# Kernel optimization log

Measured on AMD Instinct MI355X. Metric: run time of the kernel, lower is better.

## Reference

```python
import jax, jax.numpy as jnp
import numpy as np

B, N, E, ENT, D, H, L = 64, 2048, 32768, 100000, 256, 256, 512


def setup_inputs() -> dict:
    key = jax.random.key(0)
    ks = jax.random.split(key, 12)
    return {
        "neighbors": jax.random.randint(ks[0], (B, N), 0, ENT),
        "adj_row": jax.random.randint(ks[1], (B, E), 0, N),
        "adj_col": jax.random.randint(ks[2], (B, E), 0, N),
        "adj_val": jax.random.uniform(ks[3], (B, E), dtype=jnp.float32),
        "emb_table": jax.random.normal(ks[4], (ENT, D), dtype=jnp.float32),
        "W1": jax.random.normal(ks[5], (D, H), dtype=jnp.float32) * (1.0 / np.sqrt(H)),
        "b1": jax.random.normal(ks[6], (H,), dtype=jnp.float32) * 0.01,
        "W2": jax.random.normal(ks[7], (H, H), dtype=jnp.float32) * (1.0 / np.sqrt(H)),
        "b2": jax.random.normal(ks[8], (H,), dtype=jnp.float32) * 0.01,
        "fc1_w": jax.random.normal(ks[9], (H, H), dtype=jnp.float32) * (1.0 / np.sqrt(H)),
        "fc1_b": jax.random.normal(ks[10], (H,), dtype=jnp.float32) * 0.01,
        "cur_len": L,
    }


def _gcn_layer(x, W, b, adj_row, adj_col, adj_val):
    # x: [B,N,din] -> support: [B,N,dout]
    support = jnp.einsum("bnd,dh->bnh", x, W)
    # sparse adj @ support: gather columns, scale by edge value, scatter-add to rows
    gathered = jnp.take_along_axis(support, adj_col[:, :, None], axis=1)  # [B,E,h]
    weighted = gathered * adj_val[:, :, None]
    agg = jax.vmap(lambda r, g: jax.ops.segment_sum(g, r, num_segments=N))(adj_row, weighted)
    return agg + b


def reference(neighbors, adj_row, adj_col, adj_val, emb_table, W1, b1, W2, b2, fc1_w, fc1_b, cur_len):
    x = emb_table[neighbors]                                   # [B,N,D] embedding gather
    x = _gcn_layer(x, W1, b1, adj_row, adj_col, adj_val)       # GCN layer 1
    x = _gcn_layer(x, W2, b2, adj_row, adj_col, adj_val)       # GCN layer 2
    seq = x[:, :cur_len, :]                                    # keep cur_node prefix, padded to common L
    pooled = jnp.mean(seq, axis=1, keepdims=True)              # self.seq == 'mean'
    return jax.nn.relu(jnp.einsum("blh,ho->blo", pooled, fc1_w) + fc1_b)  # [B,1,H]
```

## Files before the change

kernel.cpp:

```cpp
#include <hip/hip_runtime.h>

#define B 64
#define N 2048
#define E 32768
#define D 256
#define H 256
#define GCH 32
#define SEG 8
#define EPB (E / SEG)

__global__ __launch_bounds__(512) void edge_w_kernel(
    const int* __restrict__ adj_row, const int* __restrict__ adj_col,
    const float* __restrict__ adj_val, const int* __restrict__ cur_len,
    float* __restrict__ w_part, float* __restrict__ sw_part)
{
    __shared__ float wloc[N];
    __shared__ float sred[8];
    const int b = blockIdx.x, seg = blockIdx.y, tid = threadIdx.x;
    const int L = *cur_len;

    ((float4*)wloc)[tid] = make_float4(0.f, 0.f, 0.f, 0.f);
    __syncthreads();

    const int base = b * E + seg * EPB;
    const int4*   row4 = (const int4*)  (adj_row + base);
    const int4*   col4 = (const int4*)  (adj_col + base);
    const float4* val4 = (const float4*)(adj_val + base);

    float svp = 0.f;
    #pragma unroll
    for (int k = 0; k < EPB / (512 * 4); ++k) {
        const int    i = tid + k * 512;
        const int4   r = row4[i];
        const int4   c = col4[i];
        const float4 v = val4[i];
        if (r.x < L) { atomicAdd(&wloc[c.x], v.x); svp += v.x; }
        if (r.y < L) { atomicAdd(&wloc[c.y], v.y); svp += v.y; }
        if (r.z < L) { atomicAdd(&wloc[c.z], v.z); svp += v.z; }
        if (r.w < L) { atomicAdd(&wloc[c.w], v.w); svp += v.w; }
    }
    __syncthreads();

    float4* dst = (float4*)(w_part + ((size_t)b * SEG + seg) * N);
    dst[tid] = ((const float4*)wloc)[tid];

    for (int off = 32; off; off >>= 1) svp += __shfl_down(svp, off, 64);
    if ((tid & 63) == 0) sred[tid >> 6] = svp;
    __syncthreads();
    if (tid == 0) {
        float s = 0.f;
        #pragma unroll
        for (int i = 0; i < 8; ++i) s += sred[i];
        sw_part[b * SEG + seg] = s;
    }
}

__global__ __launch_bounds__(512) void edge_z_kernel(
    const int* __restrict__ adj_row, const int* __restrict__ adj_col,
    const float* __restrict__ adj_val, const float* __restrict__ w_part,
    float* __restrict__ z_part)
{
    __shared__ float wfull[N];
    __shared__ float zloc[N];
    const int b = blockIdx.x, seg = blockIdx.y, tid = threadIdx.x;

    const float4* wp4 = (const float4*)(w_part + (size_t)b * SEG * N);
    float4 s = make_float4(0.f, 0.f, 0.f, 0.f);
    #pragma unroll
    for (int sg = 0; sg < SEG; ++sg) {
        const float4 v = wp4[sg * (N / 4) + tid];
        s.x += v.x; s.y += v.y; s.z += v.z; s.w += v.w;
    }
    ((float4*)wfull)[tid] = s;
    ((float4*)zloc)[tid]  = make_float4(0.f, 0.f, 0.f, 0.f);
    __syncthreads();

    const int base = b * E + seg * EPB;
    const int4*   row4 = (const int4*)  (adj_row + base);
    const int4*   col4 = (const int4*)  (adj_col + base);
    const float4* val4 = (const float4*)(adj_val + base);

    #pragma unroll
    for (int k = 0; k < EPB / (512 * 4); ++k) {
        const int    i = tid + k * 512;
        const int4   r = row4[i];
        const int4   c = col4[i];
        const float4 v = val4[i];
        float wv;
        wv = wfull[r.x]; if (wv != 0.f) atomicAdd(&zloc[c.x], wv * v.x);
        wv = wfull[r.y]; if (wv != 0.f) atomicAdd(&zloc[c.y], wv * v.y);
        wv = wfull[r.z]; if (wv != 0.f) atomicAdd(&zloc[c.z], wv * v.z);
        wv = wfull[r.w]; if (wv != 0.f) atomicAdd(&zloc[c.w], wv * v.w);
    }
    __syncthreads();

    float4* dst = (float4*)(z_part + ((size_t)b * SEG + seg) * N);
    dst[tid] = ((const float4*)zloc)[tid];
}

__global__ __launch_bounds__(256) void gather_kernel(
    const int* __restrict__ neighbors, const float* __restrict__ emb,
    const float* __restrict__ z_part, float* __restrict__ u_part)
{
    const int b = blockIdx.x, grp = blockIdx.y, tid = threadIdx.x;
    const int lane = tid & 63, rg = tid >> 6;
    const int n0 = grp * 64;

    __shared__ float zh[2][64];
    __shared__ int   ns[64];
    if (tid < 128) {
        const int j = tid & 63, half = tid >> 6;
        float s = 0.f;
        #pragma unroll
        for (int sg = 0; sg < SEG / 2; ++sg)
            s += z_part[((size_t)b * SEG + half * (SEG / 2) + sg) * N + n0 + j];
        zh[half][j] = s;
        if (half == 0) ns[j] = neighbors[(size_t)b * N + n0 + j];
    }
    __syncthreads();

    const float4* __restrict__ emb4 = (const float4*)emb;
    float4 a0 = make_float4(0.f,0.f,0.f,0.f), a1 = a0, a2 = a0, a3 = a0;

    #pragma unroll
    for (int i = 0; i < 16; ++i) {
        const int j = i * 4 + rg;
        const float zv = zh[0][j] + zh[1][j];
        const size_t idx = (size_t)ns[j];
        const float4 v = emb4[idx * (D / 4) + lane];
        if ((i & 3) == 0)      { a0.x += zv*v.x; a0.y += zv*v.y; a0.z += zv*v.z; a0.w += zv*v.w; }
        else if ((i & 3) == 1) { a1.x += zv*v.x; a1.y += zv*v.y; a1.z += zv*v.z; a1.w += zv*v.w; }
        else if ((i & 3) == 2) { a2.x += zv*v.x; a2.y += zv*v.y; a2.z += zv*v.z; a2.w += zv*v.w; }
        else                   { a3.x += zv*v.x; a3.y += zv*v.y; a3.z += zv*v.z; a3.w += zv*v.w; }
    }
    float4 acc = make_float4(a0.x+a1.x+a2.x+a3.x, a0.y+a1.y+a2.y+a3.y,
                             a0.z+a1.z+a2.z+a3.z, a0.w+a1.w+a2.w+a3.w);

    __shared__ float4 red[256];
    red[tid] = acc;
    __syncthreads();
    if (tid < 64) {
        float4 a = red[tid], bb = red[tid + 64], c = red[tid + 128], d = red[tid + 192];
        float4 s = make_float4(a.x + bb.x + c.x + d.x, a.y + bb.y + c.y + d.y,
                               a.z + bb.z + c.z + d.z, a.w + bb.w + c.w + d.w);
        ((float4*)u_part)[((size_t)b * GCH + grp) * (D / 4) + tid] = s;
    }
}

__global__ __launch_bounds__(1024) void head_kernel(
    const float* __restrict__ u_part, const float* __restrict__ sw_part,
    const float* __restrict__ W1, const float* __restrict__ b1,
    const float* __restrict__ W2, const float* __restrict__ b2,
    const float* __restrict__ fc1_w, const float* __restrict__ fc1_b,
    const int* __restrict__ cur_len, float* __restrict__ out)
{
    const int b = blockIdx.x;
    const int t = threadIdx.x & 255;
    const int s = threadIdx.x >> 8;
    __shared__ float red[4][256];
    __shared__ float su[D];
    __shared__ float sy[H];
    __shared__ float sp[H];

    float part = 0.f;
    #pragma unroll
    for (int c = 0; c < GCH / 4; ++c)
        part += u_part[((size_t)b * GCH + s * (GCH / 4) + c) * D + t];
    red[s][t] = part;
    __syncthreads();
    if (s == 0) su[t] = red[0][t] + red[1][t] + red[2][t] + red[3][t];
    __syncthreads();

    part = 0.f;
    #pragma unroll 8
    for (int k = 0; k < 64; ++k) {
        const int d = s * 64 + k;
        part += su[d] * W1[d * H + t];
    }
    red[s][t] = part;
    __syncthreads();
    if (s == 0) {
        float sw = 0.f;
        #pragma unroll
        for (int i = 0; i < SEG; ++i) sw += sw_part[b * SEG + i];
        sy[t] = red[0][t] + red[1][t] + red[2][t] + red[3][t] + sw * b1[t];
    }
    __syncthreads();

    const float invL = 1.f / (float)(*cur_len);
    part = 0.f;
    #pragma unroll 8
    for (int k = 0; k < 64; ++k) {
        const int d = s * 64 + k;
        part += sy[d] * W2[d * H + t];
    }
    red[s][t] = part;
    __syncthreads();
    if (s == 0)
        sp[t] = (red[0][t] + red[1][t] + red[2][t] + red[3][t]) * invL + b2[t];
    __syncthreads();

    part = 0.f;
    #pragma unroll 8
    for (int k = 0; k < 64; ++k) {
        const int d = s * 64 + k;
        part += sp[d] * fc1_w[d * H + t];
    }
    red[s][t] = part;
    __syncthreads();
    if (s == 0) {
        const float v = red[0][t] + red[1][t] + red[2][t] + red[3][t] + fc1_b[t];
        out[(size_t)b * H + t] = fmaxf(v, 0.f);
    }
}

extern "C" void kernel_launch(void* const* d_in, const int* in_sizes, int n_in,
                              void* d_out, int out_size, void* d_ws, size_t ws_size,
                              hipStream_t stream) {
    const int*   neighbors = (const int*)  d_in[0];
    const int*   adj_row   = (const int*)  d_in[1];
    const int*   adj_col   = (const int*)  d_in[2];
    const float* adj_val   = (const float*)d_in[3];
    const float* emb_table = (const float*)d_in[4];
    const float* W1        = (const float*)d_in[5];
    const float* b1        = (const float*)d_in[6];
    const float* W2        = (const float*)d_in[7];
    const float* b2        = (const float*)d_in[8];
    const float* fc1_w     = (const float*)d_in[9];
    const float* fc1_b     = (const float*)d_in[10];
    const int*   cur_len   = (const int*)  d_in[11];
    float*       out       = (float*)d_out;

    float* wp_ws = (float*)d_ws;
    float* zp_ws = wp_ws + (size_t)B * SEG * N;
    float* sw_ws = zp_ws + (size_t)B * SEG * N;
    float* u_ws  = sw_ws + (size_t)B * SEG;

    edge_w_kernel<<<dim3(B, SEG), 512, 0, stream>>>(adj_row, adj_col, adj_val,
                                                    cur_len, wp_ws, sw_ws);
    edge_z_kernel<<<dim3(B, SEG), 512, 0, stream>>>(adj_row, adj_col, adj_val,
                                                    wp_ws, zp_ws);
    gather_kernel<<<dim3(B, GCH), 256, 0, stream>>>(neighbors, emb_table, zp_ws, u_ws);
    head_kernel<<<B, 1024, 0, stream>>>(u_ws, sw_ws, W1, b1, W2, b2,
                                        fc1_w, fc1_b, cur_len, out);
}
```

Measured before the change: 222.2 us.

## Fuse edge weight and edge aggregation passes into one block per batch

Merges the two edge kernels into a single kernel in which one 1024-thread block per batch computes the row-masked column weights in shared memory and then the second-hop aggregation. This removes the per-segment partial buffers, their global reduction and one kernel launch, and simplifies the gather and head kernels. In exchange the edge work runs on only 64 blocks instead of 512, which reduces parallelism across the GPU's compute units.

```diff
diff --git a/kernel.cpp b/kernel.cpp
--- a/kernel.cpp
+++ b/kernel.cpp
@@ -6,31 +6,32 @@
 #define D 256
 #define H 256
 #define GCH 32
-#define SEG 8
-#define EPB (E / SEG)
-
-__global__ __launch_bounds__(512) void edge_w_kernel(
+
+__global__ __launch_bounds__(1024) void edges_fused_kernel(
     const int* __restrict__ adj_row, const int* __restrict__ adj_col,
     const float* __restrict__ adj_val, const int* __restrict__ cur_len,
-    float* __restrict__ w_part, float* __restrict__ sw_part)
+    float* __restrict__ z, float* __restrict__ sw)
 {
     __shared__ float wloc[N];
-    __shared__ float sred[8];
-    const int b = blockIdx.x, seg = blockIdx.y, tid = threadIdx.x;
+    __shared__ float zloc[N];
+    __shared__ float sred[16];
+    const int b = blockIdx.x, tid = threadIdx.x;
     const int L = *cur_len;
 
-    ((float4*)wloc)[tid] = make_float4(0.f, 0.f, 0.f, 0.f);
-    __syncthreads();
-
-    const int base = b * E + seg * EPB;
-    const int4*   row4 = (const int4*)  (adj_row + base);
-    const int4*   col4 = (const int4*)  (adj_col + base);
-    const float4* val4 = (const float4*)(adj_val + base);
+    if (tid < N / 4) {
+        ((float4*)wloc)[tid] = make_float4(0.f, 0.f, 0.f, 0.f);
+        ((float4*)zloc)[tid] = make_float4(0.f, 0.f, 0.f, 0.f);
+    }
+    __syncthreads();
+
+    const int4*   row4 = (const int4*)  (adj_row + (size_t)b * E);
+    const int4*   col4 = (const int4*)  (adj_col + (size_t)b * E);
+    const float4* val4 = (const float4*)(adj_val + (size_t)b * E);
 
     float svp = 0.f;
-    #pragma unroll
-    for (int k = 0; k < EPB / (512 * 4); ++k) {
-        const int    i = tid + k * 512;
+    #pragma unroll 4
+    for (int k = 0; k < E / 4 / 1024; ++k) {
+        const int    i = tid + k * 1024;
         const int4   r = row4[i];
         const int4   c = col4[i];
         const float4 v = val4[i];
@@ -39,83 +40,47 @@
         if (r.z < L) { atomicAdd(&wloc[c.z], v.z); svp += v.z; }
         if (r.w < L) { atomicAdd(&wloc[c.w], v.w); svp += v.w; }
     }
-    __syncthreads();
-
-    float4* dst = (float4*)(w_part + ((size_t)b * SEG + seg) * N);
-    dst[tid] = ((const float4*)wloc)[tid];
-
     for (int off = 32; off; off >>= 1) svp += __shfl_down(svp, off, 64);
     if ((tid & 63) == 0) sred[tid >> 6] = svp;
     __syncthreads();
-    if (tid == 0) {
-        float s = 0.f;
-        #pragma unroll
-        for (int i = 0; i < 8; ++i) s += sred[i];
-        sw_part[b * SEG + seg] = s;
-    }
-}
-
-__global__ __launch_bounds__(512) void edge_z_kernel(
-    const int* __restrict__ adj_row, const int* __restrict__ adj_col,
-    const float* __restrict__ adj_val, const float* __restrict__ w_part,
-    float* __restrict__ z_part)
-{
-    __shared__ float wfull[N];
-    __shared__ float zloc[N];
-    const int b = blockIdx.x, seg = blockIdx.y, tid = threadIdx.x;
-
-    const float4* wp4 = (const float4*)(w_part + (size_t)b * SEG * N);
-    float4 s = make_float4(0.f, 0.f, 0.f, 0.f);
-    #pragma unroll
-    for (int sg = 0; sg < SEG; ++sg) {
-        const float4 v = wp4[sg * (N / 4) + tid];
-        s.x += v.x; s.y += v.y; s.z += v.z; s.w += v.w;
-    }
-    ((float4*)wfull)[tid] = s;
-    ((float4*)zloc)[tid]  = make_float4(0.f, 0.f, 0.f, 0.f);
-    __syncthreads();
-
-    const int base = b * E + seg * EPB;
-    const int4*   row4 = (const int4*)  (adj_row + base);
-    const int4*   col4 = (const int4*)  (adj_col + base);
-    const float4* val4 = (const float4*)(adj_val + base);
-
-    #pragma unroll
-    for (int k = 0; k < EPB / (512 * 4); ++k) {
-        const int    i = tid + k * 512;
+
+    #pragma unroll 4
+    for (int k = 0; k < E / 4 / 1024; ++k) {
+        const int    i = tid + k * 1024;
         const int4   r = row4[i];
         const int4   c = col4[i];
         const float4 v = val4[i];
         float wv;
-        wv = wfull[r.x]; if (wv != 0.f) atomicAdd(&zloc[c.x], wv * v.x);
-        wv = wfull[r.y]; if (wv != 0.f) atomicAdd(&zloc[c.y], wv * v.y);
-        wv = wfull[r.z]; if (wv != 0.f) atomicAdd(&zloc[c.z], wv * v.z);
-        wv = wfull[r.w]; if (wv != 0.f) atomicAdd(&zloc[c.w], wv * v.w);
-    }
-    __syncthreads();
-
-    float4* dst = (float4*)(z_part + ((size_t)b * SEG + seg) * N);
-    dst[tid] = ((const float4*)zloc)[tid];
+        wv = wloc[r.x]; if (wv != 0.f) atomicAdd(&zloc[c.x], wv * v.x);
+        wv = wloc[r.y]; if (wv != 0.f) atomicAdd(&zloc[c.y], wv * v.y);
+        wv = wloc[r.z]; if (wv != 0.f) atomicAdd(&zloc[c.z], wv * v.z);
+        wv = wloc[r.w]; if (wv != 0.f) atomicAdd(&zloc[c.w], wv * v.w);
+    }
+    __syncthreads();
+
+    if (tid < N / 4)
+        ((float4*)(z + (size_t)b * N))[tid] = ((const float4*)zloc)[tid];
+    if (tid == 0) {
+        float s = 0.f;
+        #pragma unroll
+        for (int i = 0; i < 16; ++i) s += sred[i];
+        sw[b] = s;
+    }
 }
 
 __global__ __launch_bounds__(256) void gather_kernel(
     const int* __restrict__ neighbors, const float* __restrict__ emb,
-    const float* __restrict__ z_part, float* __restrict__ u_part)
+    const float* __restrict__ z, float* __restrict__ u_part)
 {
     const int b = blockIdx.x, grp = blockIdx.y, tid = threadIdx.x;
     const int lane = tid & 63, rg = tid >> 6;
     const int n0 = grp * 64;
 
-    __shared__ float zh[2][64];
+    __shared__ float zh[64];
     __shared__ int   ns[64];
-    if (tid < 128) {
-        const int j = tid & 63, half = tid >> 6;
-        float s = 0.f;
-        #pragma unroll
-        for (int sg = 0; sg < SEG / 2; ++sg)
-            s += z_part[((size_t)b * SEG + half * (SEG / 2) + sg) * N + n0 + j];
-        zh[half][j] = s;
-        if (half == 0) ns[j] = neighbors[(size_t)b * N + n0 + j];
+    if (tid < 64) {
+        zh[tid] = z[(size_t)b * N + n0 + tid];
+        ns[tid] = neighbors[(size_t)b * N + n0 + tid];
     }
     __syncthreads();
 
@@ -125,7 +90,7 @@
     #pragma unroll
     for (int i = 0; i < 16; ++i) {
         const int j = i * 4 + rg;
-        const float zv = zh[0][j] + zh[1][j];
+        const float zv = zh[j];
         const size_t idx = (size_t)ns[j];
         const float4 v = emb4[idx * (D / 4) + lane];
         if ((i & 3) == 0)      { a0.x += zv*v.x; a0.y += zv*v.y; a0.z += zv*v.z; a0.w += zv*v.w; }
@@ -148,7 +113,7 @@
 }
 
 __global__ __launch_bounds__(1024) void head_kernel(
-    const float* __restrict__ u_part, const float* __restrict__ sw_part,
+    const float* __restrict__ u_part, const float* __restrict__ sw_arr,
     const float* __restrict__ W1, const float* __restrict__ b1,
     const float* __restrict__ W2, const float* __restrict__ b2,
     const float* __restrict__ fc1_w, const float* __restrict__ fc1_b,
@@ -179,12 +144,8 @@
     }
     red[s][t] = part;
     __syncthreads();
-    if (s == 0) {
-        float sw = 0.f;
-        #pragma unroll
-        for (int i = 0; i < SEG; ++i) sw += sw_part[b * SEG + i];
-        sy[t] = red[0][t] + red[1][t] + red[2][t] + red[3][t] + sw * b1[t];
-    }
+    if (s == 0)
+        sy[t] = red[0][t] + red[1][t] + red[2][t] + red[3][t] + sw_arr[b] * b1[t];
     __syncthreads();
 
     const float invL = 1.f / (float)(*cur_len);
@@ -231,16 +192,13 @@
     const int*   cur_len   = (const int*)  d_in[11];
     float*       out       = (float*)d_out;
 
-    float* wp_ws = (float*)d_ws;
-    float* zp_ws = wp_ws + (size_t)B * SEG * N;
-    float* sw_ws = zp_ws + (size_t)B * SEG * N;
-    float* u_ws  = sw_ws + (size_t)B * SEG;
-
-    edge_w_kernel<<<dim3(B, SEG), 512, 0, stream>>>(adj_row, adj_col, adj_val,
-                                                    cur_len, wp_ws, sw_ws);
-    edge_z_kernel<<<dim3(B, SEG), 512, 0, stream>>>(adj_row, adj_col, adj_val,
-                                                    wp_ws, zp_ws);
-    gather_kernel<<<dim3(B, GCH), 256, 0, stream>>>(neighbors, emb_table, zp_ws, u_ws);
+    float* z_ws  = (float*)d_ws;
+    float* sw_ws = z_ws + (size_t)B * N;
+    float* u_ws  = sw_ws + B;
+
+    edges_fused_kernel<<<B, 1024, 0, stream>>>(adj_row, adj_col, adj_val,
+                                               cur_len, z_ws, sw_ws);
+    gather_kernel<<<dim3(B, GCH), 256, 0, stream>>>(neighbors, emb_table, z_ws, u_ws);
     head_kernel<<<B, 1024, 0, stream>>>(u_ws, sw_ws, W1, b1, W2, b2,
                                         fc1_w, fc1_b, cur_len, out);
 }
```

After: 257.1 us. +15.7%, slower.
